# Kernel tuning notes

Measured on AMD Instinct MI355X. Metric: run time of the kernel, lower is better.

Reference implementation:

```python
import jax, jax.numpy as jnp
import numpy as np

N_NODES = 50000
N_EDGES = 800000
HID = 128


def setup_inputs() -> dict:
    key = jax.random.key(0)
    k = jax.random.split(key, 8)
    nfeats = jax.random.normal(k[0], (N_NODES, HID), dtype=jnp.float32)
    efeats = jax.random.normal(k[1], (N_EDGES, HID), dtype=jnp.float32)
    src = jax.random.randint(k[2], (N_EDGES,), 0, N_NODES, dtype=jnp.int32)
    dst = jax.random.randint(k[3], (N_EDGES,), 0, N_NODES, dtype=jnp.int32)
    # eW: Linear(3H -> H); nW: Linear(2H -> H) (torch Linear: x @ W.T + b)
    We = jax.random.normal(k[4], (3 * HID, HID), dtype=jnp.float32) / np.sqrt(3 * HID)
    be = jnp.zeros((HID,), dtype=jnp.float32)
    Wn = jax.random.normal(k[5], (2 * HID, HID), dtype=jnp.float32) / np.sqrt(2 * HID)
    bn = jnp.zeros((HID,), dtype=jnp.float32)
    return {"nfeats": nfeats, "efeats": efeats, "src": src, "dst": dst,
            "We": We, "be": be, "Wn": Wn, "bn": bn}


def reference(nfeats, efeats, src, dst, We, be, Wn, bn):
    # --- edge message: m = ReLU(Linear(cat[src_nh, eh, dst_nh]))
    eh = jnp.concatenate([nfeats[src], efeats, nfeats[dst]], axis=-1)  # [E, 3H]
    m = jax.nn.relu(eh @ We + be)  # [E, H]
    # --- mean-reduce messages to destination nodes (DGL fn.mean: 0 for isolated nodes)
    summed = jax.ops.segment_sum(m, dst, num_segments=N_NODES)  # [N, H]
    cnt = jax.ops.segment_sum(jnp.ones((m.shape[0],), m.dtype), dst, num_segments=N_NODES)
    h = summed / jnp.maximum(cnt, 1.0)[:, None]  # [N, H]
    # --- node update: h = ReLU(Linear(cat[nh, h]))
    nh = jnp.concatenate([nfeats, h], axis=-1)  # [N, 2H]
    h_out = jax.nn.relu(nh @ Wn + bn)  # [N, H]
    # --- residuals
    return h_out + nfeats, m + efeats
```

## Files before the change

kernel.cpp:

```cpp
#include <hip/hip_runtime.h>
#include <stdint.h>

#define N_NODES 50000
#define N_EDGES 800000
#define HID 128

typedef __attribute__((ext_vector_type(8))) short bf16x8;
typedef __attribute__((ext_vector_type(4))) float f32x4;

__device__ inline uint32_t pack_bf16(float x, float y) {
    uint32_t a = __builtin_bit_cast(uint32_t, x) + 0x8000u;
    uint32_t b = __builtin_bit_cast(uint32_t, y) + 0x8000u;
    return (b & 0xffff0000u) | (a >> 16);
}

__device__ inline unsigned short cvt_bf16(float x) {
    return (unsigned short)((__builtin_bit_cast(uint32_t, x) + 0x8000u) >> 16);
}

__device__ inline bf16x8 load_row8_bf16(const float* p) {
    const float4* q = (const float4*)p;
    float4 u = q[0], v = q[1];
    union { bf16x8 v8; uint32_t u32[4]; } r;
    r.u32[0] = pack_bf16(u.x, u.y);
    r.u32[1] = pack_bf16(u.z, u.w);
    r.u32[2] = pack_bf16(v.x, v.y);
    r.u32[3] = pack_bf16(v.z, v.w);
    return r.v8;
}

__device__ inline bf16x8 load_row8_bf16_scaled(const float* p, float s) {
    const float4* q = (const float4*)p;
    float4 u = q[0], v = q[1];
    union { bf16x8 v8; uint32_t u32[4]; } r;
    r.u32[0] = pack_bf16(u.x * s, u.y * s);
    r.u32[1] = pack_bf16(u.z * s, u.w * s);
    r.u32[2] = pack_bf16(v.x * s, v.y * s);
    r.u32[3] = pack_bf16(v.z * s, v.w * s);
    return r.v8;
}

__device__ inline void gload16(const float* g, float* l) {
    __builtin_amdgcn_global_load_lds(
        (const __attribute__((address_space(1))) void*)g,
        (__attribute__((address_space(3))) void*)l, 16, 0, 0);
}

__device__ inline float lds_ef_read(const float* ef, int row, int n) {
    return ef[row * 128 + ((((n >> 2) ^ (row & 7)) << 2) | (n & 3))];
}

__device__ inline bf16x8 load_frag_lds(const float* ef, int row, int c16) {
    int s = row & 7;
    float4 u = *(const float4*)(ef + row * 128 + ((c16 ^ s) << 2));
    float4 v = *(const float4*)(ef + row * 128 + (((c16 + 1) ^ s) << 2));
    union { bf16x8 v8; uint32_t u32[4]; } r;
    r.u32[0] = pack_bf16(u.x, u.y);
    r.u32[1] = pack_bf16(u.z, u.w);
    r.u32[2] = pack_bf16(v.x, v.y);
    r.u32[3] = pack_bf16(v.z, v.w);
    return r.v8;
}

#define WE_SHUF_ELEMS (12 * 8 * 64 * 8)
#define WN_SHUF_ELEMS (8 * 8 * 64 * 8)
__global__ void prep_kernel(const float* __restrict__ We, const float* __restrict__ Wn,
                            unsigned short* __restrict__ We_shuf,
                            unsigned short* __restrict__ Wn_shuf) {
    int tid = blockIdx.x * blockDim.x + threadIdx.x;
    if (tid < WE_SHUF_ELEMS) {
        int j = tid & 7, lane = (tid >> 3) & 63, tt = tid >> 9;
        int t = tt & 7, kk = tt >> 3;
        int k = kk * 32 + (lane >> 4) * 8 + j;
        int n = t * 16 + (lane & 15);
        We_shuf[tid] = cvt_bf16(We[k * HID + n]);
    } else if (tid < WE_SHUF_ELEMS + WN_SHUF_ELEMS) {
        int id = tid - WE_SHUF_ELEMS;
        int j = id & 7, lane = (id >> 3) & 63, tt = id >> 9;
        int t = tt & 7, kk = tt >> 3;
        int k = kk * 32 + (lane >> 4) * 8 + j;
        int n = t * 16 + (lane & 15);
        Wn_shuf[id] = cvt_bf16(Wn[k * HID + n]);
    }
}

__global__ void hist_kernel(const int* __restrict__ dst, int* __restrict__ bend) {
    int e = blockIdx.x * blockDim.x + threadIdx.x;
    if (e < N_EDGES) atomicAdd(&bend[dst[e]], 1);
}

#define SCAN_T 1024
__global__ __launch_bounds__(1024) void scan_kernel(int* __restrict__ bend) {
    __shared__ int part[SCAN_T];
    int t = threadIdx.x;
    const int chunk = (N_NODES + SCAN_T - 1) / SCAN_T;
    int lo = t * chunk;
    int hi = lo + chunk;
    if (hi > N_NODES) hi = N_NODES;
    if (lo > N_NODES) lo = N_NODES;
    int s = 0;
    for (int i = lo; i < hi; ++i) s += bend[i];
    part[t] = s;
    __syncthreads();
    for (int off = 1; off < SCAN_T; off <<= 1) {
        int v = 0;
        if (t >= off) v = part[t - off];
        __syncthreads();
        if (t >= off) part[t] += v;
        __syncthreads();
    }
    int excl = (t == 0) ? 0 : part[t - 1];
    for (int i = lo; i < hi; ++i) {
        int v = bend[i];
        bend[i] = excl;
        excl += v;
    }
}

__global__ void scatter_kernel(const int* __restrict__ dst, int* __restrict__ bend,
                               int* __restrict__ order) {
    int e = blockIdx.x * blockDim.x + threadIdx.x;
    if (e < N_EDGES) {
        int pos = atomicAdd(&bend[dst[e]], 1);
        order[pos] = e;
    }
}

__global__ __launch_bounds__(128) void edge_kernel(
    const float* __restrict__ nfeats, const float* __restrict__ efeats,
    const int* __restrict__ src, const int* __restrict__ dst,
    const int* __restrict__ order,
    const unsigned short* __restrict__ We_shuf, const float* __restrict__ be,
    float* __restrict__ out1, float* __restrict__ sums) {
    __shared__ float ef_lds[2][32 * 128];
    int w = threadIdx.x >> 6;
    int wid = blockIdx.x * 2 + w;
    int lane = threadIdx.x & 63;
    int e0 = wid * 32;
    int m = lane & 15, quad = lane >> 4;
    float* ef = &ef_lds[w][0];

    int i = lane;
    int e_i = 0, d_i = 0;
    if (i < 32) {
        e_i = order[e0 + i];
        d_i = dst[e_i];
    }

#pragma unroll
    for (int it = 0; it < 16; ++it) {
        int row = 2 * it + (lane >> 5);
        int er = __shfl(e_i, row);
        int c16 = (lane & 31) ^ (row & 7);
        gload16(efeats + (size_t)er * HID + c16 * 4, ef + it * 256);
    }

    int ea = __shfl(e_i, m), eb = __shfl(e_i, 16 + m);
    int da = __shfl(d_i, m), db = __shfl(d_i, 16 + m);
    const float* s0 = nfeats + (size_t)src[ea] * HID;
    const float* s1 = nfeats + (size_t)src[eb] * HID;
    const float* d0 = nfeats + (size_t)da * HID;
    const float* d1 = nfeats + (size_t)db * HID;

    f32x4 acc[2][8];
#pragma unroll
    for (int mi = 0; mi < 2; ++mi)
#pragma unroll
        for (int t = 0; t < 8; ++t) acc[mi][t] = (f32x4){0.f, 0.f, 0.f, 0.f};

    const bf16x8* W = (const bf16x8*)We_shuf;

#pragma unroll
    for (int kk = 0; kk < 4; ++kk) {
        int off = kk * 32 + quad * 8;
        bf16x8 a0 = load_row8_bf16(s0 + off);
        bf16x8 a1 = load_row8_bf16(s1 + off);
#pragma unroll
        for (int t = 0; t < 8; ++t) {
            bf16x8 b = W[(kk * 8 + t) * 64 + lane];
            acc[0][t] = __builtin_amdgcn_mfma_f32_16x16x32_bf16(a0, b, acc[0][t], 0, 0, 0);
            acc[1][t] = __builtin_amdgcn_mfma_f32_16x16x32_bf16(a1, b, acc[1][t], 0, 0, 0);
        }
    }
#pragma unroll
    for (int kk = 8; kk < 12; ++kk) {
        int off = (kk - 8) * 32 + quad * 8;
        bf16x8 a0 = load_row8_bf16(d0 + off);
        bf16x8 a1 = load_row8_bf16(d1 + off);
#pragma unroll
        for (int t = 0; t < 8; ++t) {
            bf16x8 b = W[(kk * 8 + t) * 64 + lane];
            acc[0][t] = __builtin_amdgcn_mfma_f32_16x16x32_bf16(a0, b, acc[0][t], 0, 0, 0);
            acc[1][t] = __builtin_amdgcn_mfma_f32_16x16x32_bf16(a1, b, acc[1][t], 0, 0, 0);
        }
    }

    asm volatile("s_waitcnt vmcnt(0)" ::: "memory");

#pragma unroll
    for (int kk = 4; kk < 8; ++kk) {
        int c16 = (kk - 4) * 8 + quad * 2;
        bf16x8 a0 = load_frag_lds(ef, m, c16);
        bf16x8 a1 = load_frag_lds(ef, 16 + m, c16);
#pragma unroll
        for (int t = 0; t < 8; ++t) {
            bf16x8 b = W[(kk * 8 + t) * 64 + lane];
            acc[0][t] = __builtin_amdgcn_mfma_f32_16x16x32_bf16(a0, b, acc[0][t], 0, 0, 0);
            acc[1][t] = __builtin_amdgcn_mfma_f32_16x16x32_bf16(a1, b, acc[1][t], 0, 0, 0);
        }
    }

    float bev[8];
#pragma unroll
    for (int t = 0; t < 8; ++t) bev[t] = be[t * 16 + m];

#pragma unroll
    for (int mi = 0; mi < 2; ++mi) {
#pragma unroll
        for (int r = 0; r < 4; ++r) {
            int lrow = mi * 16 + quad * 4 + r;
            int e = __shfl(e_i, lrow);
            float* o = out1 + (size_t)e * HID;
#pragma unroll
            for (int t = 0; t < 8; ++t) {
                int n = t * 16 + m;
                float v = fmaxf(acc[mi][t][r] + bev[t], 0.0f);
                acc[mi][t][r] = v;
                o[n] = v + lds_ef_read(ef, lrow, n);
            }
        }
    }

    int dprev = __shfl(d_i, (i == 0) ? 0 : i - 1);
    bool head = (i < 32) && (i == 0 || d_i != dprev);
    unsigned long long mask = __ballot(head);
    while (mask) {
        int a = __builtin_ctzll(mask);
        mask &= mask - 1;
        int b = mask ? __builtin_ctzll(mask) : 32;
        int nd = __shfl(d_i, a);
        float tot[8];
#pragma unroll
        for (int t = 0; t < 8; ++t) tot[t] = 0.f;
#pragma unroll
        for (int mi = 0; mi < 2; ++mi) {
#pragma unroll
            for (int r = 0; r < 4; ++r) {
                int lrow = mi * 16 + quad * 4 + r;
                bool in = (lrow >= a) && (lrow < b);
#pragma unroll
                for (int t = 0; t < 8; ++t) tot[t] += in ? acc[mi][t][r] : 0.0f;
            }
        }
#pragma unroll
        for (int t = 0; t < 8; ++t) {
            tot[t] += __shfl_xor(tot[t], 16);
            tot[t] += __shfl_xor(tot[t], 32);
        }
        float* srow = sums + (size_t)nd * HID;
#pragma unroll
        for (int q = 0; q < 2; ++q) {
            int t = quad + q * 4;
            atomicAdd(&srow[t * 16 + m], tot[t]);
        }
    }
}

__global__ __launch_bounds__(256) void node_kernel(
    const float* __restrict__ nfeats, const unsigned short* __restrict__ Wn_shuf,
    const float* __restrict__ bn, const float* __restrict__ sums,
    const int* __restrict__ bend, float* __restrict__ out0) {
    int wid = blockIdx.x * 4 + (threadIdx.x >> 6);
    int n0 = wid * 16;
    if (n0 >= N_NODES) return;
    int lane = threadIdx.x & 63;
    int m = lane & 15, quad = lane >> 4;
    int row = n0 + m;
    int end = bend[row];
    int start = (row == 0) ? 0 : bend[row - 1];
    float inv = 1.0f / fmaxf((float)(end - start), 1.0f);
    const float* pn = nfeats + (size_t)row * HID;
    const float* ps = sums + (size_t)row * HID;

    f32x4 acc[8];
#pragma unroll
    for (int t = 0; t < 8; ++t) acc[t] = (f32x4){0.f, 0.f, 0.f, 0.f};

    const bf16x8* W = (const bf16x8*)Wn_shuf;

#pragma unroll
    for (int kk = 0; kk < 8; ++kk) {
        int k = kk * 32 + quad * 8;
        bf16x8 a = (k < 128) ? load_row8_bf16(pn + k)
                             : load_row8_bf16_scaled(ps + (k - 128), inv);
#pragma unroll
        for (int t = 0; t < 8; ++t) {
            bf16x8 b = W[(kk * 8 + t) * 64 + lane];
            acc[t] = __builtin_amdgcn_mfma_f32_16x16x32_bf16(a, b, acc[t], 0, 0, 0);
        }
    }

    float bnv[8];
#pragma unroll
    for (int t = 0; t < 8; ++t) bnv[t] = bn[t * 16 + m];

#pragma unroll
    for (int r = 0; r < 4; ++r) {
        int rw = n0 + quad * 4 + r;
        const float* nf = nfeats + (size_t)rw * HID;
        float* o = out0 + (size_t)rw * HID;
#pragma unroll
        for (int t = 0; t < 8; ++t) {
            int n = t * 16 + m;
            float v = fmaxf(acc[t][r] + bnv[t], 0.0f);
            o[n] = v + nf[n];
        }
    }
}

extern "C" void kernel_launch(void* const* d_in, const int* in_sizes, int n_in,
                              void* d_out, int out_size, void* d_ws, size_t ws_size,
                              hipStream_t stream) {
    const float* nfeats = (const float*)d_in[0];
    const float* efeats = (const float*)d_in[1];
    const int* src = (const int*)d_in[2];
    const int* dst = (const int*)d_in[3];
    const float* We = (const float*)d_in[4];
    const float* be = (const float*)d_in[5];
    const float* Wn = (const float*)d_in[6];
    const float* bn = (const float*)d_in[7];

    float* out0 = (float*)d_out;
    float* out1 = out0 + (size_t)N_NODES * HID;

    int* order = (int*)d_out;

    float* sums = (float*)d_ws;
    unsigned short* We_shuf = (unsigned short*)(sums + (size_t)N_NODES * HID);
    unsigned short* Wn_shuf = We_shuf + WE_SHUF_ELEMS;
    int* bend = (int*)(Wn_shuf + WN_SHUF_ELEMS);

    hipMemsetAsync(d_ws, 0,
                   (size_t)N_NODES * HID * 4 + (WE_SHUF_ELEMS + WN_SHUF_ELEMS) * 2 +
                       N_NODES * sizeof(int),
                   stream);

    prep_kernel<<<(WE_SHUF_ELEMS + WN_SHUF_ELEMS) / 256, 256, 0, stream>>>(We, Wn, We_shuf, Wn_shuf);

    hist_kernel<<<N_EDGES / 256, 256, 0, stream>>>(dst, bend);
    scan_kernel<<<1, SCAN_T, 0, stream>>>(bend);
    scatter_kernel<<<N_EDGES / 256, 256, 0, stream>>>(dst, bend, order);

    edge_kernel<<<12500, 128, 0, stream>>>(nfeats, efeats, src, dst, order,
                                           We_shuf, be, out1, sums);

    node_kernel<<<782, 256, 0, stream>>>(nfeats, Wn_shuf, bn, sums, bend, out0);
}
```

Baseline: 1.073 ms.

## Parallelize degree scan across blocks and split edge tile output columns across waves

The single-block prefix scan over node degrees is replaced by a three-kernel multi-block scan: per-block reduce, a scan of the partials, then a per-block scan with offsets. The edge kernel now has both waves of a block share one 32-edge tile, each computing half of the 128 output columns with half the accumulators, sharing an efeats LDS buffer behind a block barrier. This doubles the grid and lowers register use per wave, which may raise occupancy. In exchange, gathered node rows are loaded twice per tile (once per wave), and a barrier plus more segment atomics are added.

```diff
diff --git a/kernel.cpp b/kernel.cpp
--- a/kernel.cpp
+++ b/kernel.cpp
@@ -89,32 +89,48 @@
     if (e < N_EDGES) atomicAdd(&bend[dst[e]], 1);
 }
 
-#define SCAN_T 1024
-__global__ __launch_bounds__(1024) void scan_kernel(int* __restrict__ bend) {
-    __shared__ int part[SCAN_T];
+#define SCB 1024
+#define SCAN_NBLK ((N_NODES + SCB - 1) / SCB)
+__global__ __launch_bounds__(SCB) void scan1_kernel(const int* __restrict__ bend,
+                                                    int* __restrict__ partial) {
+    __shared__ int red[SCB];
     int t = threadIdx.x;
-    const int chunk = (N_NODES + SCAN_T - 1) / SCAN_T;
-    int lo = t * chunk;
-    int hi = lo + chunk;
-    if (hi > N_NODES) hi = N_NODES;
-    if (lo > N_NODES) lo = N_NODES;
-    int s = 0;
-    for (int i = lo; i < hi; ++i) s += bend[i];
-    part[t] = s;
+    int g = blockIdx.x * SCB + t;
+    red[t] = (g < N_NODES) ? bend[g] : 0;
     __syncthreads();
-    for (int off = 1; off < SCAN_T; off <<= 1) {
-        int v = 0;
-        if (t >= off) v = part[t - off];
+    for (int s = SCB / 2; s > 0; s >>= 1) {
+        if (t < s) red[t] += red[t + s];
         __syncthreads();
-        if (t >= off) part[t] += v;
+    }
+    if (t == 0) partial[blockIdx.x] = red[0];
+}
+
+__global__ void scan2_kernel(int* __restrict__ partial) {
+    int t = threadIdx.x;
+    int v = (t < SCAN_NBLK) ? partial[t] : 0;
+    int incl = v;
+    for (int off = 1; off < 64; off <<= 1) {
+        int u = __shfl(incl, (t >= off) ? t - off : 0);
+        if (t >= off) incl += u;
+    }
+    if (t < SCAN_NBLK) partial[t] = incl - v;
+}
+
+__global__ __launch_bounds__(SCB) void scan3_kernel(int* __restrict__ bend,
+                                                    const int* __restrict__ partial) {
+    __shared__ int sc[SCB];
+    int t = threadIdx.x;
+    int g = blockIdx.x * SCB + t;
+    int v = (g < N_NODES) ? bend[g] : 0;
+    sc[t] = v;
+    __syncthreads();
+    for (int off = 1; off < SCB; off <<= 1) {
+        int u = (t >= off) ? sc[t - off] : 0;
         __syncthreads();
-    }
-    int excl = (t == 0) ? 0 : part[t - 1];
-    for (int i = lo; i < hi; ++i) {
-        int v = bend[i];
-        bend[i] = excl;
-        excl += v;
-    }
+        sc[t] += u;
+        __syncthreads();
+    }
+    if (g < N_NODES) bend[g] = sc[t] - v + partial[blockIdx.x];
 }
 
 __global__ void scatter_kernel(const int* __restrict__ dst, int* __restrict__ bend,
@@ -126,19 +142,19 @@
     }
 }
 
-__global__ __launch_bounds__(128) void edge_kernel(
+__global__ __launch_bounds__(128, 4) void edge_kernel(
     const float* __restrict__ nfeats, const float* __restrict__ efeats,
     const int* __restrict__ src, const int* __restrict__ dst,
     const int* __restrict__ order,
     const unsigned short* __restrict__ We_shuf, const float* __restrict__ be,
     float* __restrict__ out1, float* __restrict__ sums) {
-    __shared__ float ef_lds[2][32 * 128];
+    __shared__ float ef_lds[32 * 128];
     int w = threadIdx.x >> 6;
-    int wid = blockIdx.x * 2 + w;
+    int wid = blockIdx.x;
     int lane = threadIdx.x & 63;
     int e0 = wid * 32;
     int m = lane & 15, quad = lane >> 4;
-    float* ef = &ef_lds[w][0];
+    float* ef = &ef_lds[0];
 
     int i = lane;
     int e_i = 0, d_i = 0;
@@ -148,7 +164,8 @@
     }
 
 #pragma unroll
-    for (int it = 0; it < 16; ++it) {
+    for (int it2 = 0; it2 < 8; ++it2) {
+        int it = w * 8 + it2;
         int row = 2 * it + (lane >> 5);
         int er = __shfl(e_i, row);
         int c16 = (lane & 31) ^ (row & 7);
@@ -162,13 +179,14 @@
     const float* d0 = nfeats + (size_t)da * HID;
     const float* d1 = nfeats + (size_t)db * HID;
 
-    f32x4 acc[2][8];
+    f32x4 acc[2][4];
 #pragma unroll
     for (int mi = 0; mi < 2; ++mi)
 #pragma unroll
-        for (int t = 0; t < 8; ++t) acc[mi][t] = (f32x4){0.f, 0.f, 0.f, 0.f};
+        for (int t = 0; t < 4; ++t) acc[mi][t] = (f32x4){0.f, 0.f, 0.f, 0.f};
 
     const bf16x8* W = (const bf16x8*)We_shuf;
+    int tbase = w * 4;
 
 #pragma unroll
     for (int kk = 0; kk < 4; ++kk) {
@@ -176,8 +194,8 @@
         bf16x8 a0 = load_row8_bf16(s0 + off);
         bf16x8 a1 = load_row8_bf16(s1 + off);
 #pragma unroll
-        for (int t = 0; t < 8; ++t) {
-            bf16x8 b = W[(kk * 8 + t) * 64 + lane];
+        for (int t = 0; t < 4; ++t) {
+            bf16x8 b = W[(kk * 8 + tbase + t) * 64 + lane];
             acc[0][t] = __builtin_amdgcn_mfma_f32_16x16x32_bf16(a0, b, acc[0][t], 0, 0, 0);
             acc[1][t] = __builtin_amdgcn_mfma_f32_16x16x32_bf16(a1, b, acc[1][t], 0, 0, 0);
         }
@@ -188,14 +206,15 @@
         bf16x8 a0 = load_row8_bf16(d0 + off);
         bf16x8 a1 = load_row8_bf16(d1 + off);
 #pragma unroll
-        for (int t = 0; t < 8; ++t) {
-            bf16x8 b = W[(kk * 8 + t) * 64 + lane];
+        for (int t = 0; t < 4; ++t) {
+            bf16x8 b = W[(kk * 8 + tbase + t) * 64 + lane];
             acc[0][t] = __builtin_amdgcn_mfma_f32_16x16x32_bf16(a0, b, acc[0][t], 0, 0, 0);
             acc[1][t] = __builtin_amdgcn_mfma_f32_16x16x32_bf16(a1, b, acc[1][t], 0, 0, 0);
         }
     }
 
     asm volatile("s_waitcnt vmcnt(0)" ::: "memory");
+    __syncthreads();
 
 #pragma unroll
     for (int kk = 4; kk < 8; ++kk) {
@@ -203,16 +222,16 @@
         bf16x8 a0 = load_frag_lds(ef, m, c16);
         bf16x8 a1 = load_frag_lds(ef, 16 + m, c16);
 #pragma unroll
-        for (int t = 0; t < 8; ++t) {
-            bf16x8 b = W[(kk * 8 + t) * 64 + lane];
+        for (int t = 0; t < 4; ++t) {
+            bf16x8 b = W[(kk * 8 + tbase + t) * 64 + lane];
             acc[0][t] = __builtin_amdgcn_mfma_f32_16x16x32_bf16(a0, b, acc[0][t], 0, 0, 0);
             acc[1][t] = __builtin_amdgcn_mfma_f32_16x16x32_bf16(a1, b, acc[1][t], 0, 0, 0);
         }
     }
 
-    float bev[8];
-#pragma unroll
-    for (int t = 0; t < 8; ++t) bev[t] = be[t * 16 + m];
+    float bev[4];
+#pragma unroll
+    for (int t = 0; t < 4; ++t) bev[t] = be[(tbase + t) * 16 + m];
 
 #pragma unroll
     for (int mi = 0; mi < 2; ++mi) {
@@ -222,8 +241,8 @@
             int e = __shfl(e_i, lrow);
             float* o = out1 + (size_t)e * HID;
 #pragma unroll
-            for (int t = 0; t < 8; ++t) {
-                int n = t * 16 + m;
+            for (int t = 0; t < 4; ++t) {
+                int n = (tbase + t) * 16 + m;
                 float v = fmaxf(acc[mi][t][r] + bev[t], 0.0f);
                 acc[mi][t][r] = v;
                 o[n] = v + lds_ef_read(ef, lrow, n);
@@ -239,9 +258,9 @@
         mask &= mask - 1;
         int b = mask ? __builtin_ctzll(mask) : 32;
         int nd = __shfl(d_i, a);
-        float tot[8];
-#pragma unroll
-        for (int t = 0; t < 8; ++t) tot[t] = 0.f;
+        float tot[4];
+#pragma unroll
+        for (int t = 0; t < 4; ++t) tot[t] = 0.f;
 #pragma unroll
         for (int mi = 0; mi < 2; ++mi) {
 #pragma unroll
@@ -249,20 +268,15 @@
                 int lrow = mi * 16 + quad * 4 + r;
                 bool in = (lrow >= a) && (lrow < b);
 #pragma unroll
-                for (int t = 0; t < 8; ++t) tot[t] += in ? acc[mi][t][r] : 0.0f;
+                for (int t = 0; t < 4; ++t) tot[t] += in ? acc[mi][t][r] : 0.0f;
             }
         }
 #pragma unroll
-        for (int t = 0; t < 8; ++t) {
+        for (int t = 0; t < 4; ++t) {
             tot[t] += __shfl_xor(tot[t], 16);
             tot[t] += __shfl_xor(tot[t], 32);
         }
-        float* srow = sums + (size_t)nd * HID;
-#pragma unroll
-        for (int q = 0; q < 2; ++q) {
-            int t = quad + q * 4;
-            atomicAdd(&srow[t * 16 + m], tot[t]);
-        }
+        atomicAdd(&sums[(size_t)nd * HID + (tbase + quad) * 16 + m], tot[quad]);
     }
 }
 
@@ -339,6 +353,7 @@
     unsigned short* We_shuf = (unsigned short*)(sums + (size_t)N_NODES * HID);
     unsigned short* Wn_shuf = We_shuf + WE_SHUF_ELEMS;
     int* bend = (int*)(Wn_shuf + WN_SHUF_ELEMS);
+    int* partial = bend + N_NODES;
 
     hipMemsetAsync(d_ws, 0,
                    (size_t)N_NODES * HID * 4 + (WE_SHUF_ELEMS + WN_SHUF_ELEMS) * 2 +
@@ -348,10 +363,12 @@
     prep_kernel<<<(WE_SHUF_ELEMS + WN_SHUF_ELEMS) / 256, 256, 0, stream>>>(We, Wn, We_shuf, Wn_shuf);
 
     hist_kernel<<<N_EDGES / 256, 256, 0, stream>>>(dst, bend);
-    scan_kernel<<<1, SCAN_T, 0, stream>>>(bend);
+    scan1_kernel<<<SCAN_NBLK, SCB, 0, stream>>>(bend, partial);
+    scan2_kernel<<<1, 64, 0, stream>>>(partial);
+    scan3_kernel<<<SCAN_NBLK, SCB, 0, stream>>>(bend, partial);
     scatter_kernel<<<N_EDGES / 256, 256, 0, stream>>>(dst, bend, order);
 
-    edge_kernel<<<12500, 128, 0, stream>>>(nfeats, efeats, src, dst, order,
+    edge_kernel<<<25000, 128, 0, stream>>>(nfeats, efeats, src, dst, order,
                                            We_shuf, be, out1, sums);
 
     node_kernel<<<782, 256, 0, stream>>>(nfeats, Wn_shuf, bn, sums, bend, out0);
```

Result: faster. 1.039 ms (-3.2%).
